# Kernel tuning notes

Hardware: AMD Instinct MI355X
Metric: run time of the kernel (lower is better)

## Reference

```python
import jax, jax.numpy as jnp
import numpy as np

B = 4096
C = 32000

def setup_inputs() -> dict:
    key = jax.random.key(0)
    k1, k2 = jax.random.split(key)
    output = jax.random.normal(k1, (B, C), dtype=jnp.float32)
    target = jax.random.randint(k2, (B,), 0, C, dtype=jnp.int64)
    return {"output": output, "target": target}

def reference(output, target):
    # probs: [B, C]
    probs = jax.nn.softmax(output, axis=1)
    batch_size, num_classes = probs.shape
    avg_conf = jnp.mean(probs, axis=0)  # [C]
    # avg_count[c] = mean(target == c)  == bincount(target)/B, fused scatter-add
    counts = jnp.zeros((num_classes,), dtype=probs.dtype).at[target].add(1.0)
    avg_count = counts / batch_size
    loss_mdca = jnp.mean(jnp.abs(avg_conf - avg_count))
    return loss_mdca
```

## Files before the change

### kernel.cpp

```cpp
#include <hip/hip_runtime.h>

#define BB 4096
#define CC 32000
#define NCHUNK 16
#define ROWS_PER_CHUNK (BB / NCHUNK)

__global__ __launch_bounds__(256) void row_sumexp(const float* __restrict__ x,
                                                  float* __restrict__ rcpZ) {
    const int row = blockIdx.x;
    const int t = threadIdx.x;
    const float4* rp4 = (const float4*)(x + (size_t)row * CC);
    float s = 0.f;
    for (int i = t; i < CC / 4; i += 256) {
        float4 v = rp4[i];
        s += __expf(v.x) + __expf(v.y) + __expf(v.z) + __expf(v.w);
    }
    for (int off = 32; off > 0; off >>= 1) s += __shfl_down(s, off);
    __shared__ float wsum[4];
    if ((t & 63) == 0) wsum[t >> 6] = s;
    __syncthreads();
    if (t == 0) {
        float tot = wsum[0] + wsum[1] + wsum[2] + wsum[3];
        rcpZ[row] = 1.0f / tot;
    }
}

__global__ __launch_bounds__(256) void col_partial(const float* __restrict__ x,
                                                   const float* __restrict__ rcpZ,
                                                   float* __restrict__ partial) {
    const int c = blockIdx.x * 256 + threadIdx.x;
    const int b0 = blockIdx.y * ROWS_PER_CHUNK;
    __shared__ float rz[ROWS_PER_CHUNK];
    for (int i = threadIdx.x; i < ROWS_PER_CHUNK; i += 256) rz[i] = rcpZ[b0 + i];
    __syncthreads();
    const float* p = x + (size_t)b0 * CC + c;
    float acc = 0.f;
#pragma unroll 4
    for (int i = 0; i < ROWS_PER_CHUNK; ++i) {
        acc += __expf(p[(size_t)i * CC]) * rz[i];
    }
    partial[(size_t)blockIdx.y * CC + c] = acc;
}

__global__ void bincount_k(const int* __restrict__ tgt, float* __restrict__ counts) {
    int i = blockIdx.x * 256 + threadIdx.x;
    if (i < BB) atomicAdd(&counts[tgt[i]], 1.0f);
}

__global__ __launch_bounds__(256) void finalize(const float* __restrict__ partial,
                                                const float* __restrict__ counts,
                                                float* __restrict__ out) {
    const int c = blockIdx.x * 256 + threadIdx.x;
    float s = 0.f;
#pragma unroll
    for (int k = 0; k < NCHUNK; ++k) s += partial[(size_t)k * CC + c];
    float v = fabsf(s - counts[c]) * (1.0f / BB);
    for (int off = 32; off > 0; off >>= 1) v += __shfl_down(v, off);
    __shared__ float wsum[4];
    const int t = threadIdx.x;
    if ((t & 63) == 0) wsum[t >> 6] = v;
    __syncthreads();
    if (t == 0) {
        float tot = (wsum[0] + wsum[1] + wsum[2] + wsum[3]) * (1.0f / CC);
        atomicAdd(out, tot);
    }
}

extern "C" void kernel_launch(void* const* d_in, const int* in_sizes, int n_in,
                              void* d_out, int out_size, void* d_ws, size_t ws_size,
                              hipStream_t stream) {
    const float* x = (const float*)d_in[0];
    const int* tgt = (const int*)d_in[1];
    float* out = (float*)d_out;

    float* counts = (float*)d_ws;
    float* rcpZ = counts + CC;
    float* partial = rcpZ + BB;

    hipMemsetAsync(counts, 0, CC * sizeof(float), stream);
    hipMemsetAsync(d_out, 0, sizeof(float), stream);

    bincount_k<<<(BB + 255) / 256, 256, 0, stream>>>(tgt, counts);
    row_sumexp<<<BB, 256, 0, stream>>>(x, rcpZ);
    col_partial<<<dim3(CC / 256, NCHUNK), 256, 0, stream>>>(x, rcpZ, partial);
    finalize<<<CC / 256, 256, 0, stream>>>(partial, counts, out);
}
```

Measured before the change: 752.0 us.

## Stash exp values as fp8 in row pass to shrink column-pass traffic

The row pass now computes exp once, writes a packed fp8 (e4m3) copy of exp(x) to workspace, and also does the target bincount. The column pass reads the 4x smaller stash instead of re-reading and re-exponentiating the fp32 input, with wider per-thread vectors. Finalize uses a completion counter so the last block writes the scaled result, which removes a memset. The cost is extra workspace writes and quantisation error in the column sums, which could affect accuracy of the small loss value.

```diff
diff --git a/kernel.cpp b/kernel.cpp
--- a/kernel.cpp
+++ b/kernel.cpp
@@ -2,67 +2,130 @@
 
 #define BB 4096
 #define CC 32000
-#define NCHUNK 16
-#define ROWS_PER_CHUNK (BB / NCHUNK)
+#define W32 8000
+#define W64 4000
+#define NCHUNK 64
+#define RPC (BB / NCHUNK)
+#define FBLK 125
 
-__global__ __launch_bounds__(256) void row_sumexp(const float* __restrict__ x,
-                                                  float* __restrict__ rcpZ) {
+typedef float v2f __attribute__((ext_vector_type(2)));
+typedef float v4f __attribute__((ext_vector_type(4)));
+
+#if defined(__has_builtin)
+#if __has_builtin(__builtin_amdgcn_cvt_pk_fp8_f32) && __has_builtin(__builtin_amdgcn_cvt_pk_f32_fp8)
+#define HW_FP8 1
+#endif
+#endif
+
+#ifndef HW_FP8
+__device__ inline unsigned sw_enc(float v) {
+    if (v < 0.015625f) return (unsigned)__float2int_rn(v * 512.0f);
+    unsigned u = __float_as_uint(v);
+    unsigned m = (u >> 20) & 7;
+    unsigned rest = u & 0xfffff;
+    int e32 = (int)((u >> 23) & 0xff);
+    if (rest > 0x80000 || (rest == 0x80000 && (m & 1))) { if (++m == 8) { m = 0; e32++; } }
+    int ee = e32 - 127 + 7;
+    if (ee > 15) { ee = 15; m = 6; }
+    return ((unsigned)ee << 3) | m;
+}
+__device__ inline float sw_dec(unsigned b) {
+    unsigned e = (b >> 3) & 0xf, m = b & 7;
+    if (e == 0) return (float)m * 0.001953125f;
+    return __uint_as_float(((e - 7 + 127) << 23) | (m << 20));
+}
+#endif
+
+__global__ __launch_bounds__(256) void row_pass(const float* __restrict__ x,
+                                                const int* __restrict__ tgt,
+                                                unsigned* __restrict__ stash,
+                                                float* __restrict__ rcpZ,
+                                                float* __restrict__ counts) {
     const int row = blockIdx.x;
     const int t = threadIdx.x;
-    const float4* rp4 = (const float4*)(x + (size_t)row * CC);
+    const v4f* rp4 = (const v4f*)(x + (size_t)row * CC);
+    unsigned* sp = stash + (size_t)row * W32;
     float s = 0.f;
-    for (int i = t; i < CC / 4; i += 256) {
-        float4 v = rp4[i];
-        s += __expf(v.x) + __expf(v.y) + __expf(v.z) + __expf(v.w);
+    for (int i = t; i < W32; i += 256) {
+        v4f v = __builtin_nontemporal_load(&rp4[i]);
+        float e0 = __expf(v.x), e1 = __expf(v.y), e2 = __expf(v.z), e3 = __expf(v.w);
+        s += e0 + e1 + e2 + e3;
+#ifdef HW_FP8
+        int w = __builtin_amdgcn_cvt_pk_fp8_f32(fminf(e0, 440.f), fminf(e1, 440.f), 0, false);
+        w = __builtin_amdgcn_cvt_pk_fp8_f32(fminf(e2, 440.f), fminf(e3, 440.f), w, true);
+        sp[i] = (unsigned)w;
+#else
+        sp[i] = sw_enc(fminf(e0, 440.f)) | (sw_enc(fminf(e1, 440.f)) << 8) |
+                (sw_enc(fminf(e2, 440.f)) << 16) | (sw_enc(fminf(e3, 440.f)) << 24);
+#endif
     }
     for (int off = 32; off > 0; off >>= 1) s += __shfl_down(s, off);
     __shared__ float wsum[4];
     if ((t & 63) == 0) wsum[t >> 6] = s;
     __syncthreads();
     if (t == 0) {
-        float tot = wsum[0] + wsum[1] + wsum[2] + wsum[3];
-        rcpZ[row] = 1.0f / tot;
+        rcpZ[row] = 1.0f / (wsum[0] + wsum[1] + wsum[2] + wsum[3]);
+        atomicAdd(&counts[tgt[row]], 1.0f);
     }
 }
 
-__global__ __launch_bounds__(256) void col_partial(const float* __restrict__ x,
-                                                   const float* __restrict__ rcpZ,
-                                                   float* __restrict__ partial) {
-    const int c = blockIdx.x * 256 + threadIdx.x;
-    const int b0 = blockIdx.y * ROWS_PER_CHUNK;
-    __shared__ float rz[ROWS_PER_CHUNK];
-    for (int i = threadIdx.x; i < ROWS_PER_CHUNK; i += 256) rz[i] = rcpZ[b0 + i];
+__global__ __launch_bounds__(256) void col_pass(const uint2* __restrict__ stash,
+                                                const float* __restrict__ rcpZ,
+                                                float* __restrict__ partial) {
+    const int g = blockIdx.x * 256 + threadIdx.x;
+    const int b0 = blockIdx.y * RPC;
+    __shared__ float rz[RPC];
+    if (threadIdx.x < RPC) rz[threadIdx.x] = rcpZ[b0 + threadIdx.x];
     __syncthreads();
-    const float* p = x + (size_t)b0 * CC + c;
-    float acc = 0.f;
+    if (g >= W64) return;
+    float a0 = 0, a1 = 0, a2 = 0, a3 = 0, a4 = 0, a5 = 0, a6 = 0, a7 = 0;
+    const uint2* p = stash + (size_t)b0 * W64 + g;
 #pragma unroll 4
-    for (int i = 0; i < ROWS_PER_CHUNK; ++i) {
-        acc += __expf(p[(size_t)i * CC]) * rz[i];
+    for (int i = 0; i < RPC; ++i) {
+        uint2 w = p[(size_t)i * W64];
+        float r = rz[i];
+#ifdef HW_FP8
+        v2f f01 = __builtin_amdgcn_cvt_pk_f32_fp8((int)w.x, false);
+        v2f f23 = __builtin_amdgcn_cvt_pk_f32_fp8((int)w.x, true);
+        v2f f45 = __builtin_amdgcn_cvt_pk_f32_fp8((int)w.y, false);
+        v2f f67 = __builtin_amdgcn_cvt_pk_f32_fp8((int)w.y, true);
+        a0 += f01.x * r; a1 += f01.y * r; a2 += f23.x * r; a3 += f23.y * r;
+        a4 += f45.x * r; a5 += f45.y * r; a6 += f67.x * r; a7 += f67.y * r;
+#else
+        a0 += sw_dec(w.x & 0xff) * r;         a1 += sw_dec((w.x >> 8) & 0xff) * r;
+        a2 += sw_dec((w.x >> 16) & 0xff) * r; a3 += sw_dec(w.x >> 24) * r;
+        a4 += sw_dec(w.y & 0xff) * r;         a5 += sw_dec((w.y >> 8) & 0xff) * r;
+        a6 += sw_dec((w.y >> 16) & 0xff) * r; a7 += sw_dec(w.y >> 24) * r;
+#endif
     }
-    partial[(size_t)blockIdx.y * CC + c] = acc;
-}
-
-__global__ void bincount_k(const int* __restrict__ tgt, float* __restrict__ counts) {
-    int i = blockIdx.x * 256 + threadIdx.x;
-    if (i < BB) atomicAdd(&counts[tgt[i]], 1.0f);
+    float* d = partial + (size_t)blockIdx.y * CC + (size_t)g * 8;
+    float4 o0 = {a0, a1, a2, a3}, o1 = {a4, a5, a6, a7};
+    ((float4*)d)[0] = o0;
+    ((float4*)d)[1] = o1;
 }
 
 __global__ __launch_bounds__(256) void finalize(const float* __restrict__ partial,
                                                 const float* __restrict__ counts,
+                                                float* __restrict__ total,
+                                                unsigned* __restrict__ blkcnt,
                                                 float* __restrict__ out) {
     const int c = blockIdx.x * 256 + threadIdx.x;
     float s = 0.f;
 #pragma unroll
     for (int k = 0; k < NCHUNK; ++k) s += partial[(size_t)k * CC + c];
-    float v = fabsf(s - counts[c]) * (1.0f / BB);
+    float v = fabsf(s - counts[c]);
     for (int off = 32; off > 0; off >>= 1) v += __shfl_down(v, off);
     __shared__ float wsum[4];
-    const int t = threadIdx.x;
-    if ((t & 63) == 0) wsum[t >> 6] = v;
+    if ((threadIdx.x & 63) == 0) wsum[threadIdx.x >> 6] = v;
     __syncthreads();
-    if (t == 0) {
-        float tot = (wsum[0] + wsum[1] + wsum[2] + wsum[3]) * (1.0f / CC);
-        atomicAdd(out, tot);
+    if (threadIdx.x == 0) {
+        atomicAdd(total, wsum[0] + wsum[1] + wsum[2] + wsum[3]);
+        __threadfence();
+        unsigned prev = atomicAdd(blkcnt, 1u);
+        if (prev == FBLK - 1) {
+            float tot = atomicAdd(total, 0.0f);
+            out[0] = tot * (1.0f / ((float)BB * (float)CC));
+        }
     }
 }
 
@@ -73,15 +136,17 @@
     const int* tgt = (const int*)d_in[1];
     float* out = (float*)d_out;
 
-    float* counts = (float*)d_ws;
-    float* rcpZ = counts + CC;
-    float* partial = rcpZ + BB;
+    char* base = (char*)d_ws;
+    unsigned* stash = (unsigned*)base;
+    float* partial = (float*)(base + (size_t)BB * W32 * 4);
+    float* counts = (float*)(base + (size_t)BB * W32 * 4 + (size_t)NCHUNK * CC * 4);
+    float* total = counts + CC;
+    unsigned* blkcnt = (unsigned*)(total + 1);
+    float* rcpZ = (float*)(blkcnt + 1);
 
-    hipMemsetAsync(counts, 0, CC * sizeof(float), stream);
-    hipMemsetAsync(d_out, 0, sizeof(float), stream);
+    (void)hipMemsetAsync(counts, 0, (size_t)(CC + 2) * 4, stream);
 
-    bincount_k<<<(BB + 255) / 256, 256, 0, stream>>>(tgt, counts);
-    row_sumexp<<<BB, 256, 0, stream>>>(x, rcpZ);
-    col_partial<<<dim3(CC / 256, NCHUNK), 256, 0, stream>>>(x, rcpZ, partial);
-    finalize<<<CC / 256, 256, 0, stream>>>(partial, counts, out);
+    row_pass<<<BB, 256, 0, stream>>>(x, tgt, stash, rcpZ, counts);
+    col_pass<<<dim3((W64 + 255) / 256, NCHUNK), 256, 0, stream>>>((const uint2*)stash, rcpZ, partial);
+    finalize<<<FBLK, 256, 0, stream>>>(partial, counts, total, blkcnt, out);
 }
```

New measurement: 712.3 us. 5.3% less time.

## Fuse row softmax normalization and column accumulation into single-pass LDS kernel

Applied to the files above, without the earlier changes.

Replaces the separate row-sum and column-sum kernels with one kernel in which each block streams its rows once, computes exp and the row normalizer in registers, and accumulates normalized probabilities into a full-width LDS column buffer. This halves the reads of the large input. Bincount is folded into the main kernel, and finalize uses a last-block counter to write the result. Costs are heavy LDS use (128KB per block), large register arrays with possible spills, two barriers per row, and a larger partials buffer to reduce.

```diff
diff --git a/kernel.cpp b/kernel.cpp
--- a/kernel.cpp
+++ b/kernel.cpp
@@ -2,67 +2,128 @@
 
 #define BB 4096
 #define CC 32000
-#define NCHUNK 16
-#define ROWS_PER_CHUNK (BB / NCHUNK)
+#define CPAD 32768
+#define NT 512
+#define NI 16
+#define GRID 256
+#define RPB (BB / GRID)
+#define FBLK 128
 
-__global__ __launch_bounds__(256) void row_sumexp(const float* __restrict__ x,
-                                                  float* __restrict__ rcpZ) {
-    const int row = blockIdx.x;
+typedef float v4f __attribute__((ext_vector_type(4)));
+
+__global__ __launch_bounds__(NT, 2) void mdca_main(const float* __restrict__ x,
+                                                   const int* __restrict__ tgt,
+                                                   float* __restrict__ partial,
+                                                   float* __restrict__ counts) {
+    __shared__ float acc[CPAD];
+    __shared__ float red[NT / 64];
+    __shared__ float s_rcp;
+
     const int t = threadIdx.x;
-    const float4* rp4 = (const float4*)(x + (size_t)row * CC);
-    float s = 0.f;
-    for (int i = t; i < CC / 4; i += 256) {
-        float4 v = rp4[i];
-        s += __expf(v.x) + __expf(v.y) + __expf(v.z) + __expf(v.w);
+    const int r0 = blockIdx.x * RPB;
+
+    for (int i = t; i < CPAD / 4; i += NT) ((v4f*)acc)[i] = (v4f){0.f, 0.f, 0.f, 0.f};
+
+    v4f cur[NI], nxt[NI];
+
+    {
+        const float* rp = x + (size_t)r0 * CC;
+#pragma unroll
+        for (int i = 0; i < NI; ++i) {
+            const int col = i * 2048 + 4 * t;
+            if (col < CC) cur[i] = __builtin_nontemporal_load((const v4f*)(rp + col));
+        }
     }
-    for (int off = 32; off > 0; off >>= 1) s += __shfl_down(s, off);
-    __shared__ float wsum[4];
-    if ((t & 63) == 0) wsum[t >> 6] = s;
     __syncthreads();
-    if (t == 0) {
-        float tot = wsum[0] + wsum[1] + wsum[2] + wsum[3];
-        rcpZ[row] = 1.0f / tot;
+
+    for (int r = 0; r < RPB; ++r) {
+        if (r + 1 < RPB) {
+            const float* rp = x + (size_t)(r0 + r + 1) * CC;
+#pragma unroll
+            for (int i = 0; i < NI; ++i) {
+                const int col = i * 2048 + 4 * t;
+                if (col < CC) nxt[i] = __builtin_nontemporal_load((const v4f*)(rp + col));
+            }
+        }
+        float s = 0.f;
+#pragma unroll
+        for (int i = 0; i < NI; ++i) {
+            const int col = i * 2048 + 4 * t;
+            if (col < CC) {
+                v4f e;
+                e.x = __expf(cur[i].x); e.y = __expf(cur[i].y);
+                e.z = __expf(cur[i].z); e.w = __expf(cur[i].w);
+                cur[i] = e;
+                s += e.x + e.y + e.z + e.w;
+            }
+        }
+        for (int off = 32; off > 0; off >>= 1) s += __shfl_down(s, off);
+        if ((t & 63) == 0) red[t >> 6] = s;
+        __syncthreads();
+        if (t == 0) {
+            float z = 0.f;
+#pragma unroll
+            for (int w = 0; w < NT / 64; ++w) z += red[w];
+            s_rcp = 1.0f / z;
+        }
+        __syncthreads();
+        const float rz = s_rcp;
+#pragma unroll
+        for (int i = 0; i < NI; ++i) {
+            const int col = i * 2048 + 4 * t;
+            if (col < CC) {
+                v4f a = ((v4f*)acc)[i * 512 + t];
+                a.x += cur[i].x * rz; a.y += cur[i].y * rz;
+                a.z += cur[i].z * rz; a.w += cur[i].w * rz;
+                ((v4f*)acc)[i * 512 + t] = a;
+            }
+        }
+        if (r + 1 < RPB) {
+#pragma unroll
+            for (int i = 0; i < NI; ++i) cur[i] = nxt[i];
+        }
     }
-}
 
-__global__ __launch_bounds__(256) void col_partial(const float* __restrict__ x,
-                                                   const float* __restrict__ rcpZ,
-                                                   float* __restrict__ partial) {
-    const int c = blockIdx.x * 256 + threadIdx.x;
-    const int b0 = blockIdx.y * ROWS_PER_CHUNK;
-    __shared__ float rz[ROWS_PER_CHUNK];
-    for (int i = threadIdx.x; i < ROWS_PER_CHUNK; i += 256) rz[i] = rcpZ[b0 + i];
-    __syncthreads();
-    const float* p = x + (size_t)b0 * CC + c;
-    float acc = 0.f;
-#pragma unroll 4
-    for (int i = 0; i < ROWS_PER_CHUNK; ++i) {
-        acc += __expf(p[(size_t)i * CC]) * rz[i];
+    v4f* pp = (v4f*)(partial + (size_t)blockIdx.x * CPAD);
+#pragma unroll
+    for (int i = 0; i < NI; ++i) {
+        const int col = i * 2048 + 4 * t;
+        v4f a = (col < CC) ? ((v4f*)acc)[i * 512 + t] : (v4f){0.f, 0.f, 0.f, 0.f};
+        pp[i * 512 + t] = a;
     }
-    partial[(size_t)blockIdx.y * CC + c] = acc;
-}
-
-__global__ void bincount_k(const int* __restrict__ tgt, float* __restrict__ counts) {
-    int i = blockIdx.x * 256 + threadIdx.x;
-    if (i < BB) atomicAdd(&counts[tgt[i]], 1.0f);
+    if (t < RPB) atomicAdd(&counts[tgt[r0 + t]], 1.0f);
 }
 
 __global__ __launch_bounds__(256) void finalize(const float* __restrict__ partial,
                                                 const float* __restrict__ counts,
+                                                float* __restrict__ total,
+                                                unsigned* __restrict__ blkcnt,
                                                 float* __restrict__ out) {
-    const int c = blockIdx.x * 256 + threadIdx.x;
-    float s = 0.f;
-#pragma unroll
-    for (int k = 0; k < NCHUNK; ++k) s += partial[(size_t)k * CC + c];
-    float v = fabsf(s - counts[c]) * (1.0f / BB);
+    const int g = blockIdx.x * 256 + threadIdx.x;
+    v4f s = {0.f, 0.f, 0.f, 0.f};
+    const v4f* pv = (const v4f*)partial;
+    for (int b = 0; b < GRID; ++b) {
+        v4f p = pv[(size_t)b * (CPAD / 4) + g];
+        s.x += p.x; s.y += p.y; s.z += p.z; s.w += p.w;
+    }
+    float v = 0.f;
+    const int c = 4 * g;
+    if (c < CC) {
+        v4f cnt = *(const v4f*)(counts + c);
+        v = fabsf(s.x - cnt.x) + fabsf(s.y - cnt.y) + fabsf(s.z - cnt.z) + fabsf(s.w - cnt.w);
+    }
     for (int off = 32; off > 0; off >>= 1) v += __shfl_down(v, off);
     __shared__ float wsum[4];
-    const int t = threadIdx.x;
-    if ((t & 63) == 0) wsum[t >> 6] = v;
+    if ((threadIdx.x & 63) == 0) wsum[threadIdx.x >> 6] = v;
     __syncthreads();
-    if (t == 0) {
-        float tot = (wsum[0] + wsum[1] + wsum[2] + wsum[3]) * (1.0f / CC);
-        atomicAdd(out, tot);
+    if (threadIdx.x == 0) {
+        atomicAdd(total, wsum[0] + wsum[1] + wsum[2] + wsum[3]);
+        __threadfence();
+        unsigned prev = atomicAdd(blkcnt, 1u);
+        if (prev == FBLK - 1) {
+            float tot = atomicAdd(total, 0.0f);
+            out[0] = tot * (1.0f / ((float)BB * (float)CC));
+        }
     }
 }
 
@@ -73,15 +134,13 @@
     const int* tgt = (const int*)d_in[1];
     float* out = (float*)d_out;
 
-    float* counts = (float*)d_ws;
-    float* rcpZ = counts + CC;
-    float* partial = rcpZ + BB;
+    float* partial = (float*)d_ws;
+    float* counts = partial + (size_t)GRID * CPAD;
+    float* total = counts + CC;
+    unsigned* blkcnt = (unsigned*)(total + 1);
 
-    hipMemsetAsync(counts, 0, CC * sizeof(float), stream);
-    hipMemsetAsync(d_out, 0, sizeof(float), stream);
+    (void)hipMemsetAsync(counts, 0, (size_t)(CC + 2) * 4, stream);
 
-    bincount_k<<<(BB + 255) / 256, 256, 0, stream>>>(tgt, counts);
-    row_sumexp<<<BB, 256, 0, stream>>>(x, rcpZ);
-    col_partial<<<dim3(CC / 256, NCHUNK), 256, 0, stream>>>(x, rcpZ, partial);
-    finalize<<<CC / 256, 256, 0, stream>>>(partial, counts, out);
+    mdca_main<<<GRID, NT, 0, stream>>>(x, tgt, partial, counts);
+    finalize<<<FBLK, 256, 0, stream>>>(partial, counts, total, blkcnt, out);
 }
```

Result: faster. 659.1 us (-12.4%).
